# Performance work log

Measured on AMD Instinct MI355X. Metric: run time of the kernel, lower is better.

The kernel has to match this reference:

```python
import jax, jax.numpy as jnp
import numpy as np


def _dct2_basis(N, K):
    # Unnormalized DCT-II basis as used by torch_dct.dct(norm=None):
    #   X_k = 2 * sum_n x_n * cos(pi * (2n+1) * k / (2N))
    # Returns [K, N]: only the first K (low-frequency) rows are needed.
    n = jnp.arange(N, dtype=jnp.float32)
    k = jnp.arange(K, dtype=jnp.float32)
    return 2.0 * jnp.cos(jnp.pi * (2.0 * n[None, :] + 1.0) * k[:, None] / (2.0 * N))


def setup_inputs() -> dict:
    key = jax.random.key(0)
    x = jax.random.normal(key, (16, 64, 256, 256), dtype=jnp.float32)
    return {"x": x, "num_coeffs": 32}


def reference(x, num_coeffs):
    # x: [B, C, H, W]. Equivalent to dct.dct_2d(x)[:, :, :K, :K] (norm=None),
    # computed directly via truncated cosine-basis GEMMs.
    B, C, H, W = x.shape
    Ch = _dct2_basis(H, num_coeffs)  # [K, H]
    Cw = _dct2_basis(W, num_coeffs)  # [K, W]
    # [B, C, K, K] = Ch @ x @ Cw^T over the last two dims
    return jnp.einsum('kh,bchw,lw->bckl', Ch, x, Cw)
```

## Files before the change

### kernel.cpp

```cpp
#include <hip/hip_runtime.h>
#include <math.h>
#include <string.h>

#define KC 32

typedef __attribute__((ext_vector_type(8))) short bf16x8;
typedef __attribute__((ext_vector_type(4))) float f32x4;

__device__ __forceinline__ unsigned pack2_bf16(float a, float b) {
    unsigned ua = __float_as_uint(a); ua += 0x7fffu + ((ua >> 16) & 1u);
    unsigned ub = __float_as_uint(b); ub += 0x7fffu + ((ub >> 16) & 1u);
    return (ua >> 16) | (ub & 0xffff0000u);
}

static unsigned short h_tab[8192];
static const bool h_tab_ready = []() {
    for (int t = 0; t < 1024; ++t) {
        int c = t >> 7, sub = (t >> 6) & 1, lane = t & 63;
        int g = lane >> 4, cl = lane & 15;
        for (int i = 0; i < 8; ++i) {
            int A = 32 * c + 8 * g + i;
            int B = sub * 16 + cl;
            double v = 2.0 * cos(M_PI * (double)(2 * A + 1) * (double)B / 512.0);
            float f = (float)v;
            unsigned u;
            memcpy(&u, &f, 4);
            u += 0x7fffu + ((u >> 16) & 1u);
            h_tab[t * 8 + i] = (unsigned short)(u >> 16);
        }
    }
    return true;
}();

__global__ __launch_bounds__(256, 3) void dct_trunc_kernel(
    const float* __restrict__ x, float* __restrict__ out,
    const unsigned short* __restrict__ tab) {
    __shared__ uint4 ldsbuf[2560];
    char* lds = (char*)ldsbuf;
    const bf16x8* __restrict__ tabv = (const bf16x8*)tab;

    const int tid  = threadIdx.x;
    const int lane = tid & 63;
    const int wv   = tid >> 6;
    const int g    = lane >> 4;
    const int cl   = lane & 15;
    const int img  = blockIdx.x;
    const float* __restrict__ xi = x + (size_t)img * 65536;

    const int srow = tid >> 3;
    const int sc   = tid & 7;

    const float* __restrict__ sbase = xi + (size_t)srow * 256 + sc * 4;
    char* const wbase = lds + srow * 80 + sc * 8;

    float4 pf[8], qf[8];

    auto stage_load = [&](float4 (&P)[8], int c_) {
        const float* s_ = sbase + (size_t)c_ * 32;
        #pragma unroll
        for (int j = 0; j < 8; ++j)
            P[j] = *(const float4*)(s_ + j * 8192);
    };
    auto stage_write = [&](const float4 (&P)[8], int base_) {
        char* b_ = wbase + base_;
        #pragma unroll
        for (int j = 0; j < 8; ++j)
            *(uint2*)(b_ + j * 2560) =
                make_uint2(pack2_bf16(P[j].x, P[j].y), pack2_bf16(P[j].z, P[j].w));
    };

    f32x4 a00 = {0.f,0.f,0.f,0.f}, a01 = a00, a10 = a00, a11 = a00;
    f32x4 a20 = a00, a21 = a00, a30 = a00, a31 = a00;

    stage_load(pf, 0);
    stage_write(pf, 0);
    stage_load(pf, 1);
    stage_load(qf, 2);

    const int frow = cl * 80 + g * 16;

    #pragma unroll
    for (int c = 0; c < 8; ++c) {
        __syncthreads();

        if (c < 7) {
            if ((c & 1) == 0) stage_write(pf, ((c + 1) & 1) * 20480);
            else              stage_write(qf, ((c + 1) & 1) * 20480);
        }
        if (c < 5) {
            if ((c & 1) == 0) stage_load(pf, c + 3);
            else              stage_load(qf, c + 3);
        }

        bf16x8 bf0 = tabv[(c * 2 + 0) * 64 + lane];
        bf16x8 bf1 = tabv[(c * 2 + 1) * 64 + lane];

        const char* xb = lds + (c & 1) * 20480;
        bf16x8 xf0 = *(const bf16x8*)(xb + (wv +  0) * 1280 + frow);
        bf16x8 xf1 = *(const bf16x8*)(xb + (wv +  4) * 1280 + frow);
        bf16x8 xf2 = *(const bf16x8*)(xb + (wv +  8) * 1280 + frow);
        bf16x8 xf3 = *(const bf16x8*)(xb + (wv + 12) * 1280 + frow);

        a00 = __builtin_amdgcn_mfma_f32_16x16x32_bf16(xf0, bf0, a00, 0, 0, 0);
        a01 = __builtin_amdgcn_mfma_f32_16x16x32_bf16(xf0, bf1, a01, 0, 0, 0);
        a10 = __builtin_amdgcn_mfma_f32_16x16x32_bf16(xf1, bf0, a10, 0, 0, 0);
        a11 = __builtin_amdgcn_mfma_f32_16x16x32_bf16(xf1, bf1, a11, 0, 0, 0);
        a20 = __builtin_amdgcn_mfma_f32_16x16x32_bf16(xf2, bf0, a20, 0, 0, 0);
        a21 = __builtin_amdgcn_mfma_f32_16x16x32_bf16(xf2, bf1, a21, 0, 0, 0);
        a30 = __builtin_amdgcn_mfma_f32_16x16x32_bf16(xf3, bf0, a30, 0, 0, 0);
        a31 = __builtin_amdgcn_mfma_f32_16x16x32_bf16(xf3, bf1, a31, 0, 0, 0);
    }

    auto utw = [&](int q_, const f32x4& A0, const f32x4& A1) {
        char* u0 = lds + (0 * 16 + cl) * 528 + (wv + 4 * q_) * 32 + g * 8;
        char* u1 = lds + (1 * 16 + cl) * 528 + (wv + 4 * q_) * 32 + g * 8;
        *(uint2*)u0 = make_uint2(pack2_bf16(A0[0], A0[1]), pack2_bf16(A0[2], A0[3]));
        *(uint2*)u1 = make_uint2(pack2_bf16(A1[0], A1[1]), pack2_bf16(A1[2], A1[3]));
    };
    utw(0, a00, a01);
    utw(1, a10, a11);
    utw(2, a20, a21);
    utw(3, a30, a31);
    __syncthreads();

    const int mt2 = wv >> 1;
    const int nt2 = wv & 1;
    f32x4 acc2 = {0.f, 0.f, 0.f, 0.f};
    const char* ub = lds + (nt2 * 16 + cl) * 528 + g * 16;
    #pragma unroll
    for (int c2 = 0; c2 < 8; ++c2) {
        bf16x8 af = tabv[(c2 * 2 + mt2) * 64 + lane];
        bf16x8 uf = *(const bf16x8*)(ub + c2 * 64);
        acc2 = __builtin_amdgcn_mfma_f32_16x16x32_bf16(af, uf, acc2, 0, 0, 0);
    }

    float* op = out + (size_t)img * 1024 + (mt2 * 16 + g * 4) * 32 + nt2 * 16 + cl;
    op[0]  = acc2[0];
    op[32] = acc2[1];
    op[64] = acc2[2];
    op[96] = acc2[3];
}

extern "C" void kernel_launch(void* const* d_in, const int* in_sizes, int n_in,
                              void* d_out, int out_size, void* d_ws, size_t ws_size,
                              hipStream_t stream) {
    const float* x = (const float*)d_in[0];
    float* out = (float*)d_out;
    unsigned short* tab = (unsigned short*)d_ws;

    (void)h_tab_ready;
    hipMemcpyAsync(tab, h_tab, sizeof(h_tab), hipMemcpyHostToDevice, stream);

    const int n_imgs = in_sizes[0] / 65536;
    dct_trunc_kernel<<<n_imgs, 256, 0, stream>>>(x, out, tab);
}
```

Measured before the change: 51.06 us.

## Use hardware bf16 pack, single register stage, and raise occupancy to 4

Swaps the software round-to-nearest bf16 packing for the v_cvt_pk_bf16_f32 instruction. It also drops the second prefetch register buffer, so only the next chunk is loaded, after the sync, and written to LDS after the MFMAs. Launch bounds go from 3 to 4 waves per SIMD. The loop is only partly unrolled. Fewer registers should allow more resident blocks to hide memory latency, but the prefetch now runs one stage ahead instead of three, which shortens latency hiding within a block.

```diff
diff --git a/kernel.cpp b/kernel.cpp
--- a/kernel.cpp
+++ b/kernel.cpp
@@ -7,10 +7,10 @@
 typedef __attribute__((ext_vector_type(8))) short bf16x8;
 typedef __attribute__((ext_vector_type(4))) float f32x4;
 
-__device__ __forceinline__ unsigned pack2_bf16(float a, float b) {
-    unsigned ua = __float_as_uint(a); ua += 0x7fffu + ((ua >> 16) & 1u);
-    unsigned ub = __float_as_uint(b); ub += 0x7fffu + ((ub >> 16) & 1u);
-    return (ua >> 16) | (ub & 0xffff0000u);
+__device__ __forceinline__ unsigned cvt_pk_bf16(float a, float b) {
+    unsigned r;
+    asm("v_cvt_pk_bf16_f32 %0, %1, %2" : "=v"(r) : "v"(a), "v"(b));
+    return r;
 }
 
 static unsigned short h_tab[8192];
@@ -32,7 +32,7 @@
     return true;
 }();
 
-__global__ __launch_bounds__(256, 3) void dct_trunc_kernel(
+__global__ __launch_bounds__(256, 4) void dct_trunc_kernel(
     const float* __restrict__ x, float* __restrict__ out,
     const unsigned short* __restrict__ tab) {
     __shared__ uint4 ldsbuf[2560];
@@ -51,46 +51,37 @@
     const int sc   = tid & 7;
 
     const float* __restrict__ sbase = xi + (size_t)srow * 256 + sc * 4;
-    char* const wbase = lds + srow * 80 + sc * 8;
+    char* const wb_ = lds + srow * 80 + sc * 8;
 
-    float4 pf[8], qf[8];
+    float4 pf[8];
 
-    auto stage_load = [&](float4 (&P)[8], int c_) {
+    auto stage_load = [&](int c_) {
         const float* s_ = sbase + (size_t)c_ * 32;
         #pragma unroll
         for (int j = 0; j < 8; ++j)
-            P[j] = *(const float4*)(s_ + j * 8192);
+            pf[j] = *(const float4*)(s_ + j * 8192);
     };
-    auto stage_write = [&](const float4 (&P)[8], int base_) {
-        char* b_ = wbase + base_;
+    auto stage_write = [&](int base_) {
+        char* b_ = wb_ + base_;
         #pragma unroll
         for (int j = 0; j < 8; ++j)
             *(uint2*)(b_ + j * 2560) =
-                make_uint2(pack2_bf16(P[j].x, P[j].y), pack2_bf16(P[j].z, P[j].w));
+                make_uint2(cvt_pk_bf16(pf[j].x, pf[j].y), cvt_pk_bf16(pf[j].z, pf[j].w));
     };
 
     f32x4 a00 = {0.f,0.f,0.f,0.f}, a01 = a00, a10 = a00, a11 = a00;
     f32x4 a20 = a00, a21 = a00, a30 = a00, a31 = a00;
 
-    stage_load(pf, 0);
-    stage_write(pf, 0);
-    stage_load(pf, 1);
-    stage_load(qf, 2);
+    stage_load(0);
+    stage_write(0);
 
     const int frow = cl * 80 + g * 16;
 
-    #pragma unroll
+    #pragma unroll 2
     for (int c = 0; c < 8; ++c) {
         __syncthreads();
 
-        if (c < 7) {
-            if ((c & 1) == 0) stage_write(pf, ((c + 1) & 1) * 20480);
-            else              stage_write(qf, ((c + 1) & 1) * 20480);
-        }
-        if (c < 5) {
-            if ((c & 1) == 0) stage_load(pf, c + 3);
-            else              stage_load(qf, c + 3);
-        }
+        if (c < 7) stage_load(c + 1);
 
         bf16x8 bf0 = tabv[(c * 2 + 0) * 64 + lane];
         bf16x8 bf1 = tabv[(c * 2 + 1) * 64 + lane];
@@ -109,13 +100,15 @@
         a21 = __builtin_amdgcn_mfma_f32_16x16x32_bf16(xf2, bf1, a21, 0, 0, 0);
         a30 = __builtin_amdgcn_mfma_f32_16x16x32_bf16(xf3, bf0, a30, 0, 0, 0);
         a31 = __builtin_amdgcn_mfma_f32_16x16x32_bf16(xf3, bf1, a31, 0, 0, 0);
+
+        if (c < 7) stage_write(((c + 1) & 1) * 20480);
     }
 
     auto utw = [&](int q_, const f32x4& A0, const f32x4& A1) {
         char* u0 = lds + (0 * 16 + cl) * 528 + (wv + 4 * q_) * 32 + g * 8;
         char* u1 = lds + (1 * 16 + cl) * 528 + (wv + 4 * q_) * 32 + g * 8;
-        *(uint2*)u0 = make_uint2(pack2_bf16(A0[0], A0[1]), pack2_bf16(A0[2], A0[3]));
-        *(uint2*)u1 = make_uint2(pack2_bf16(A1[0], A1[1]), pack2_bf16(A1[2], A1[3]));
+        *(uint2*)u0 = make_uint2(cvt_pk_bf16(A0[0], A0[1]), cvt_pk_bf16(A0[2], A0[3]));
+        *(uint2*)u1 = make_uint2(cvt_pk_bf16(A1[0], A1[1]), cvt_pk_bf16(A1[2], A1[3]));
     };
     utw(0, a00, a01);
     utw(1, a10, a11);
```

Result: no change. 50.52 us (-1.1%).
